# Optimization experiments

Hardware: AMD Instinct MI355X
Metric: run time of the kernel (lower is better)

## Reference

```python
import jax, jax.numpy as jnp
import numpy as np

B, S, HID = 1, 2048, 4096
H, KH, D = 32, 8, 128          # query heads, kv heads, head_dim
ROT = 64                       # rotary_dim = head_dim * partial_rotary_factor (0.5)
THETA = 10000.0
EPS = 1e-5
SCALE = D ** -0.5
NEG = -1e30


def setup_inputs() -> dict:
    key = jax.random.key(0)
    ks = jax.random.split(key, 7)
    return {
        "hidden_states": jax.random.normal(ks[0], (B, S, HID), jnp.float32),
        "Wq": jax.random.normal(ks[1], (H * D, HID), jnp.float32) * 0.02,
        "Wk": jax.random.normal(ks[2], (KH * D, HID), jnp.float32) * 0.02,
        "Wv": jax.random.normal(ks[3], (KH * D, HID), jnp.float32) * 0.02,
        "Wo": jax.random.normal(ks[4], (H * D, HID), jnp.float32).T.reshape(HID, H * D) * 0.02,
        "q_norm_w": jax.random.uniform(ks[5], (D,), jnp.float32),
        "k_norm_w": jax.random.uniform(ks[6], (D,), jnp.float32),
        "position_ids": jnp.arange(S, dtype=jnp.int32)[None, :],
    }


def rms_norm(x, w):
    # per-head RMSNorm in fp32, scale by (weight + 1)
    xf = x.astype(jnp.float32)
    var = jnp.mean(xf * xf, axis=-1, keepdims=True)
    return (xf * jax.lax.rsqrt(var + EPS) * (w.astype(jnp.float32) + 1.0)).astype(x.dtype)


def rope_cos_sin(position_ids):
    inv_freq = 1.0 / (THETA ** (jnp.arange(0, ROT, 2, dtype=jnp.float32) / ROT))
    freqs = position_ids.astype(jnp.float32)[..., None] * inv_freq  # [B,S,ROT/2]
    emb = jnp.concatenate([freqs, freqs], axis=-1)                  # [B,S,ROT]
    return jnp.cos(emb)[:, None], jnp.sin(emb)[:, None]             # [B,1,S,ROT]


def rotate_half(x):
    x1, x2 = jnp.split(x, 2, axis=-1)
    return jnp.concatenate([-x2, x1], axis=-1)


def apply_partial_rope(x, cos, sin):
    x_rot, x_pass = x[..., :ROT], x[..., ROT:]
    x_rot = x_rot * cos + rotate_half(x_rot) * sin
    return jnp.concatenate([x_rot, x_pass], axis=-1)


def reference(hidden_states, Wq, Wk, Wv, Wo, q_norm_w, k_norm_w, position_ids):
    # projections -> [B, heads, S, D]
    q = (hidden_states @ Wq.T).reshape(B, S, H, D).transpose(0, 2, 1, 3)
    k = (hidden_states @ Wk.T).reshape(B, S, KH, D).transpose(0, 2, 1, 3)
    v = (hidden_states @ Wv.T).reshape(B, S, KH, D).transpose(0, 2, 1, 3)

    q = rms_norm(q, q_norm_w)
    k = rms_norm(k, k_norm_w)

    cos, sin = rope_cos_sin(position_ids)
    q = apply_partial_rope(q, cos, sin)
    k = apply_partial_rope(k, cos, sin)

    # repeat kv heads (GQA) -> [B, H, S, D]
    rep = H // KH
    k = jnp.broadcast_to(k[:, :, None], (B, KH, rep, S, D)).reshape(B, H, S, D)
    v = jnp.broadcast_to(v[:, :, None], (B, KH, rep, S, D)).reshape(B, H, S, D)

    scores = jnp.einsum("bhqd,bhkd->bhqk", q, k) * SCALE
    causal = jnp.tril(jnp.ones((S, S), bool))
    scores = jnp.where(causal, scores, NEG)
    attn = jax.nn.softmax(scores, axis=-1)
    out = jnp.einsum("bhqk,bhkd->bhqd", attn, v)        # [B,H,S,D]
    out = out.transpose(0, 2, 1, 3).reshape(B, S, H * D)
    return out @ Wo.T                                    # [B,S,HID]
```

## Files before the change

### kernel.cpp

```cpp
#include <hip/hip_runtime.h>
#include <hip/hip_bf16.h>

#define AS1 __attribute__((address_space(1)))
#define AS3 __attribute__((address_space(3)))

typedef __attribute__((ext_vector_type(8))) short short8;
typedef __attribute__((ext_vector_type(4))) short short4v;
typedef __attribute__((ext_vector_type(4))) float f32x4;

constexpr int S_ = 2048;
constexpr int HID_ = 4096;
constexpr int NH = 32;
constexpr int NKH = 8;
constexpr float EPS_ = 1e-5f;
constexpr float SCALE_ = 0.08838834764831845f;

__device__ __forceinline__ short f2bf(float f) {
  __hip_bfloat16 h = __float2bfloat16(f);
  return *reinterpret_cast<short*>(&h);
}

__global__ __launch_bounds__(256) void cast_bf16_kernel(const float4* __restrict__ src,
                                                        short4v* __restrict__ dst, int n4) {
  int i = blockIdx.x * 256 + threadIdx.x;
  if (i >= n4) return;
  float4 v = src[i];
  short4v o;
  o[0] = f2bf(v.x); o[1] = f2bf(v.y); o[2] = f2bf(v.z); o[3] = f2bf(v.w);
  dst[i] = o;
}

__global__ __launch_bounds__(512, 2) void gemm8_bt(const short* __restrict__ A,
                                                   const short* __restrict__ B,
                                                   float* __restrict__ C,
                                                   int M, int N, int K) {
  extern __shared__ __align__(16) char smem[];
  const int t = threadIdx.x, w = t >> 6, lane = t & 63;
  const int nbx = N >> 8;
  int wg = blockIdx.x;
  const int cpx = gridDim.x >> 3;
  wg = (wg & 7) * cpx + (wg >> 3);
  const int by = wg / nbx, bx = wg % nbx;
  const long m0 = (long)by << 8, n0 = (long)bx << 8;
  const int wr = w >> 2, wc = w & 3;
  const int l15 = lane & 15, l4 = lane >> 4;
  const int NT = K >> 6;

  f32x4 acc[8][4];
#pragma unroll
  for (int f = 0; f < 8; ++f)
#pragma unroll
    for (int g = 0; g < 4; ++g) acc[f][g] = (f32x4){0.f, 0.f, 0.f, 0.f};

  auto STAGE = [&](int h) {
    int hm = h & (4 * NT - 1);
    int tt = hm >> 2, half = hm & 3;
    int buf = tt & 1;
    long k0 = (long)tt << 6;
    const short* src = (half < 2) ? A : B;
    long r0 = (half < 2) ? m0 : n0;
    char* lbase = smem + buf * 65536 + ((half >> 1) << 15) + ((half & 1) << 14);
#pragma unroll
    for (int j = 0; j < 2; ++j) {
      int row = ((half & 1) << 7) + j * 64 + w * 8 + (lane >> 3);
      int cs = (lane & 7) ^ (((row >> 2) & 1) << 1);
      __builtin_amdgcn_global_load_lds(
          (const AS1 void*)(src + (r0 + row) * K + k0 + cs * 8),
          (AS3 void*)(lbase + j * 8192 + w * 1024 + lane * 16), 16, 0, 0);
    }
  };
  auto LDA = [&](int buf, int f, int s) -> short8 {
    int ra = wr * 128 + f * 16 + l15;
    int byte = (ra * 128 + s * 64 + l4 * 16) ^ (((ra >> 2) & 1) << 5);
    return *(const short8*)(smem + buf * 65536 + byte);
  };
  auto LDB = [&](int buf, int g, int s) -> short8 {
    int rb = wc * 64 + g * 16 + l15;
    int byte = (rb * 128 + s * 64 + l4 * 16) ^ (((rb >> 2) & 1) << 5);
    return *(const short8*)(smem + buf * 65536 + 32768 + byte);
  };

#pragma unroll
  for (int h = 0; h < 8; ++h) STAGE(h);
  asm volatile("s_waitcnt vmcnt(8)" ::: "memory");
  asm volatile("s_barrier" ::: "memory");

  short8 af[4][2], bf2[4][2];
  for (int tt = 0; tt < NT; ++tt) {
    const int buf = tt & 1;
    const int p = tt * 4;
#pragma unroll
    for (int f = 0; f < 4; ++f) { af[f][0] = LDA(buf, f, 0); af[f][1] = LDA(buf, f, 1); }
#pragma unroll
    for (int g = 0; g < 2; ++g) { bf2[g][0] = LDB(buf, g, 0); bf2[g][1] = LDB(buf, g, 1); }
    if (tt) STAGE(p + 5);
    asm volatile("s_barrier" ::: "memory");
    __builtin_amdgcn_s_setprio(1);
#pragma unroll
    for (int f = 0; f < 4; ++f)
#pragma unroll
      for (int g = 0; g < 2; ++g) {
        acc[f][g] = __builtin_amdgcn_mfma_f32_16x16x32_bf16(af[f][0], bf2[g][0], acc[f][g], 0, 0, 0);
        acc[f][g] = __builtin_amdgcn_mfma_f32_16x16x32_bf16(af[f][1], bf2[g][1], acc[f][g], 0, 0, 0);
      }
    __builtin_amdgcn_s_setprio(0);
    asm volatile("s_barrier" ::: "memory");
#pragma unroll
    for (int g = 0; g < 2; ++g) { bf2[2 + g][0] = LDB(buf, 2 + g, 0); bf2[2 + g][1] = LDB(buf, 2 + g, 1); }
    if (tt) STAGE(p + 6);
    asm volatile("s_barrier" ::: "memory");
    __builtin_amdgcn_s_setprio(1);
#pragma unroll
    for (int f = 0; f < 4; ++f)
#pragma unroll
      for (int g = 0; g < 2; ++g) {
        acc[f][2 + g] = __builtin_amdgcn_mfma_f32_16x16x32_bf16(af[f][0], bf2[2 + g][0], acc[f][2 + g], 0, 0, 0);
        acc[f][2 + g] = __builtin_amdgcn_mfma_f32_16x16x32_bf16(af[f][1], bf2[2 + g][1], acc[f][2 + g], 0, 0, 0);
      }
    __builtin_amdgcn_s_setprio(0);
    asm volatile("s_barrier" ::: "memory");
#pragma unroll
    for (int f = 0; f < 4; ++f) { af[f][0] = LDA(buf, 4 + f, 0); af[f][1] = LDA(buf, 4 + f, 1); }
    if (tt) STAGE(p + 7);
    asm volatile("s_barrier" ::: "memory");
    __builtin_amdgcn_s_setprio(1);
#pragma unroll
    for (int f = 0; f < 4; ++f)
#pragma unroll
      for (int g = 0; g < 2; ++g) {
        acc[4 + f][g] = __builtin_amdgcn_mfma_f32_16x16x32_bf16(af[f][0], bf2[g][0], acc[4 + f][g], 0, 0, 0);
        acc[4 + f][g] = __builtin_amdgcn_mfma_f32_16x16x32_bf16(af[f][1], bf2[g][1], acc[4 + f][g], 0, 0, 0);
      }
    __builtin_amdgcn_s_setprio(0);
    asm volatile("s_barrier" ::: "memory");
    STAGE(p + 8);
    asm volatile("s_barrier" ::: "memory");
    __builtin_amdgcn_s_setprio(1);
#pragma unroll
    for (int f = 0; f < 4; ++f)
#pragma unroll
      for (int g = 0; g < 2; ++g) {
        acc[4 + f][2 + g] = __builtin_amdgcn_mfma_f32_16x16x32_bf16(af[f][0], bf2[2 + g][0], acc[4 + f][2 + g], 0, 0, 0);
        acc[4 + f][2 + g] = __builtin_amdgcn_mfma_f32_16x16x32_bf16(af[f][1], bf2[2 + g][1], acc[4 + f][2 + g], 0, 0, 0);
      }
    __builtin_amdgcn_s_setprio(0);
    asm volatile("s_waitcnt vmcnt(2)" ::: "memory");
    asm volatile("s_barrier" ::: "memory");
  }
#pragma unroll
  for (int f = 0; f < 8; ++f)
#pragma unroll
    for (int g = 0; g < 4; ++g)
#pragma unroll
      for (int r = 0; r < 4; ++r) {
        long m = m0 + wr * 128 + f * 16 + l4 * 4 + r;
        long n = n0 + wc * 64 + g * 16 + l15;
        C[m * N + n] = acc[f][g][r];
      }
}

__global__ __launch_bounds__(256) void normrope_kernel(const float* __restrict__ QKV,
    const int* __restrict__ pos_ids, const float* __restrict__ qw,
    const float* __restrict__ kw,
    short* __restrict__ Qn, short* __restrict__ Kn) {
  const int lane = threadIdx.x & 63;
  const long row = (long)blockIdx.x * 4 + (threadIdx.x >> 6);
  const long NQ = (long)S_ * NH;
  const float* src;
  short* dst;
  const float* wv;
  int s;
  float scl = 1.f;
  if (row < NQ) {
    s = (int)(row >> 5); int h = (int)(row & 31);
    src = QKV + (long)s * 6144 + h * 128;
    dst = Qn + ((long)h * S_ + s) * 128;
    wv = qw; scl = SCALE_;
  } else {
    long r2 = row - NQ; s = (int)(r2 >> 3); int kh = (int)(r2 & 7);
    src = QKV + (long)s * 6144 + 4096 + kh * 128;
    dst = Kn + ((long)kh * S_ + s) * 128;
    wv = kw;
  }
  float x0 = src[lane], x1 = src[lane + 64];
  float ss = x0 * x0 + x1 * x1;
#pragma unroll
  for (int m = 1; m < 64; m <<= 1) ss += __shfl_xor(ss, m);
  float inv = rsqrtf(ss * (1.f / 128.f) + EPS_);
  x0 = x0 * inv * (wv[lane] + 1.f);
  x1 = x1 * inv * (wv[lane + 64] + 1.f);
  int pos = pos_ids[s];
  int i = lane & 31;
  float invf = expf(-logf(10000.f) * ((float)(2 * i) / 64.f));
  float f = (float)pos * invf;
  float c = cosf(f), sn = sinf(f);
  float p = __shfl_xor(x0, 32);
  x0 = (lane < 32) ? (x0 * c - p * sn) : (x0 * c + p * sn);
  dst[lane] = f2bf(x0 * scl);
  dst[lane + 64] = f2bf(x1 * scl);
}

__global__ __launch_bounds__(256) void vtrans_kernel(const float* __restrict__ QKV,
                                                     short* __restrict__ Vt) {
  __shared__ __align__(16) float lt[64][68];
  const int t = threadIdx.x;
  const int s0 = blockIdx.x * 64, d0 = blockIdx.y * 64, kh = blockIdx.z;
  const float* src = QKV + (long)s0 * 6144 + 5120 + kh * 128 + d0;
#pragma unroll
  for (int i = 0; i < 4; ++i) {
    int idx = t + i * 256;
    int r = idx >> 4, c4 = (idx & 15) * 4;
    float4 v = *(const float4*)(src + (long)r * 6144 + c4);
    *(float4*)&lt[r][c4] = v;
  }
  __syncthreads();
  int d = t >> 2, seg = (t & 3) * 16;
  short* dst = Vt + ((long)kh * 128 + d0 + d) * S_ + s0 + seg;
  short8 a, b2;
#pragma unroll
  for (int j = 0; j < 8; ++j) a[j] = f2bf(lt[seg + j][d]);
#pragma unroll
  for (int j = 0; j < 8; ++j) b2[j] = f2bf(lt[seg + 8 + j][d]);
  *(short8*)dst = a;
  *(short8*)(dst + 8) = b2;
}

__global__ __launch_bounds__(512, 2) void attn_kernel(const short* __restrict__ Qn,
    const short* __restrict__ Kn, const short* __restrict__ Vt,
    short* __restrict__ O) {
  __shared__ __align__(16) short Ks[64 * 128];
  __shared__ __align__(16) short Vs[128 * 64];
  __shared__ __align__(16) short Ps[8][16 * 64];
  const int t = threadIdx.x, w = t >> 6, lane = t & 63;
  const int b = blockIdx.x;
  const int h = b & 31, qt = 15 - (b >> 5);
  const int kh = h >> 2;
  const int q0 = qt * 128;
  const int l15 = lane & 15, lk = (lane >> 4) * 8;

  short8 qf[4];
  {
    const short* Qh = Qn + ((long)h * S_ + q0 + w * 16) * 128;
#pragma unroll
    for (int ks = 0; ks < 4; ++ks)
      qf[ks] = *(const short8*)(Qh + l15 * 128 + ks * 32 + lk);
  }
  f32x4 o[8];
#pragma unroll
  for (int nf = 0; nf < 8; ++nf) o[nf] = (f32x4){0.f, 0.f, 0.f, 0.f};
  float mrun[4], lrun[4];
#pragma unroll
  for (int r = 0; r < 4; ++r) { mrun[r] = -1e30f; lrun[r] = 0.f; }

  const short* Khp = Kn + (long)kh * S_ * 128;
  const short* Vtp = Vt + (long)kh * 128 * S_;

  const int krr = w * 8 + (lane >> 4);
  const int kc = lane & 15;
  const int vdd = w * 16 + (lane >> 3);
  const int vc = lane & 7;
  char* pw = (char*)Ps[w];
  const int mrow = (lane >> 4) * 4;

  for (int kv0 = 0; kv0 < q0 + 128; kv0 += 64) {
#pragma unroll
    for (int j = 0; j < 2; ++j) {
      int rr = krr + j * 4;
      __builtin_amdgcn_global_load_lds(
          (const AS1 void*)(Khp + (long)(kv0 + rr) * 128 + ((kc ^ (rr & 7)) * 8)),
          (AS3 void*)(Ks + (w * 8 + j * 4) * 128 + lane * 8), 16, 0, 0);
    }
#pragma unroll
    for (int j = 0; j < 2; ++j) {
      int d = vdd + j * 8;
      __builtin_amdgcn_global_load_lds(
          (const AS1 void*)(Vtp + (long)d * S_ + kv0 + ((vc ^ (d & 7)) * 8)),
          (AS3 void*)(Vs + (w * 16 + j * 8) * 64 + lane * 8), 16, 0, 0);
    }
    __syncthreads();

    const bool active = (kv0 <= q0 + w * 16 + 15);
    if (active) {
      f32x4 sc[4];
#pragma unroll
      for (int ni = 0; ni < 4; ++ni) sc[ni] = (f32x4){0.f, 0.f, 0.f, 0.f};
#pragma unroll
      for (int ks = 0; ks < 4; ++ks)
#pragma unroll
        for (int ni = 0; ni < 4; ++ni) {
          int row = ni * 16 + l15;
          int bb = row * 256 + (ks * 32 + lk) * 2; bb ^= (row & 7) << 4;
          short8 kf = *(const short8*)((const char*)Ks + bb);
          sc[ni] = __builtin_amdgcn_mfma_f32_16x16x32_bf16(qf[ks], kf, sc[ni], 0, 0, 0);
        }
      if (kv0 + 64 > q0 + w * 16) {
#pragma unroll
        for (int ni = 0; ni < 4; ++ni)
#pragma unroll
          for (int r = 0; r < 4; ++r) {
            int qm = q0 + w * 16 + mrow + r;
            int kcol = kv0 + ni * 16 + l15;
            if (kcol > qm) sc[ni][r] = -1e30f;
          }
      }
      short pb[4][4];
#pragma unroll
      for (int r = 0; r < 4; ++r) {
        float mx = fmaxf(fmaxf(sc[0][r], sc[1][r]), fmaxf(sc[2][r], sc[3][r]));
        mx = fmaxf(mx, __shfl_xor(mx, 1));
        mx = fmaxf(mx, __shfl_xor(mx, 2));
        mx = fmaxf(mx, __shfl_xor(mx, 4));
        mx = fmaxf(mx, __shfl_xor(mx, 8));
        float mnew = fmaxf(mrun[r], mx);
        float scale = expf(mrun[r] - mnew);
        mrun[r] = mnew;
        float ssum = 0.f;
#pragma unroll
        for (int ni = 0; ni < 4; ++ni) {
          float p = expf(sc[ni][r] - mnew);
          ssum += p;
          pb[ni][r] = f2bf(p);
        }
        ssum += __shfl_xor(ssum, 1);
        ssum += __shfl_xor(ssum, 2);
        ssum += __shfl_xor(ssum, 4);
        ssum += __shfl_xor(ssum, 8);
        lrun[r] = lrun[r] * scale + ssum;
#pragma unroll
        for (int nf = 0; nf < 8; ++nf) o[nf][r] *= scale;
      }
#pragma unroll
      for (int ni = 0; ni < 4; ++ni)
#pragma unroll
        for (int r = 0; r < 4; ++r) {
          int m = mrow + r;
          int bb = m * 128 + (ni * 16 + l15) * 2; bb ^= (m & 7) << 4;
          *(short*)(pw + bb) = pb[ni][r];
        }
#pragma unroll
      for (int ks2 = 0; ks2 < 2; ++ks2) {
        int bp = l15 * 128 + (ks2 * 32 + lk) * 2; bp ^= (l15 & 7) << 4;
        short8 pf = *(const short8*)(pw + bp);
#pragma unroll
        for (int nf = 0; nf < 8; ++nf) {
          int bv = (nf * 16 + l15) * 128 + (ks2 * 32 + lk) * 2; bv ^= (l15 & 7) << 4;
          short8 vf = *(const short8*)((const char*)Vs + bv);
          o[nf] = __builtin_amdgcn_mfma_f32_16x16x32_bf16(pf, vf, o[nf], 0, 0, 0);
        }
      }
    }
    __syncthreads();
  }
#pragma unroll
  for (int r = 0; r < 4; ++r) {
    float invl = 1.f / lrun[r];
    int m = q0 + w * 16 + mrow + r;
#pragma unroll
    for (int nf = 0; nf < 8; ++nf)
      O[(long)m * 4096 + h * 128 + nf * 16 + l15] = f2bf(o[nf][r] * invl);
  }
}

extern "C" void kernel_launch(void* const* d_in, const int* in_sizes, int n_in,
                              void* d_out, int out_size, void* d_ws, size_t ws_size,
                              hipStream_t stream) {
  const float* hidden = (const float*)d_in[0];
  const float* Wq = (const float*)d_in[1];
  const float* Wk = (const float*)d_in[2];
  const float* Wv = (const float*)d_in[3];
  const float* Wo = (const float*)d_in[4];
  const float* qw = (const float*)d_in[5];
  const float* kw = (const float*)d_in[6];
  const int* pos = (const int*)d_in[7];
  float* out = (float*)d_out;

  char* ws = (char*)d_ws;
  short* hid_bf  = (short*)(ws + 0);
  short* Wqkv_bf = (short*)(ws + 16777216L);
  short* Wo_bf   = (short*)(ws + 67108864L);
  float* QKVf    = (float*)(ws + 100663296L);
  short* Qn      = (short*)(ws + 150994944L);
  short* Kn      = (short*)(ws + 167772160L);
  short* Vt      = (short*)(ws + 171966464L);
  short* AO      = hid_bf;

  (void)hipFuncSetAttribute((const void*)gemm8_bt,
                            hipFuncAttributeMaxDynamicSharedMemorySize, 131072);

  auto cast = [&](const float* s_, short* d_, long n) {
    int n4 = (int)(n / 4);
    cast_bf16_kernel<<<(n4 + 255) / 256, 256, 0, stream>>>((const float4*)s_, (short4v*)d_, n4);
  };
  cast(hidden, hid_bf, (long)S_ * HID_);
  cast(Wq, Wqkv_bf, (long)4096 * 4096);
  cast(Wk, Wqkv_bf + (long)4096 * 4096, (long)1024 * 4096);
  cast(Wv, Wqkv_bf + (long)5120 * 4096, (long)1024 * 4096);
  cast(Wo, Wo_bf, (long)4096 * 4096);

  gemm8_bt<<<dim3(192), 512, 131072, stream>>>(hid_bf, Wqkv_bf, QKVf, S_, 6144, HID_);

  normrope_kernel<<<(S_ * (NH + NKH)) / 4, 256, 0, stream>>>(QKVf, pos, qw, kw, Qn, Kn);
  vtrans_kernel<<<dim3(S_ / 64, 2, NKH), 256, 0, stream>>>(QKVf, Vt);
  attn_kernel<<<dim3(512), 512, 0, stream>>>(Qn, Kn, Vt, AO);

  gemm8_bt<<<dim3(128), 512, 131072, stream>>>(AO, Wo_bf, out, S_, HID_, HID_);
}
```

Measured before the change: 602.8 us.

## Template GEMM on N-tile width to fill all CUs with 256 workgroups

The bf16 GEMM is templated on the N tile width (G*64 columns). The QKV projection now uses 256x192 tiles and the output projection 256x128 tiles, so both launch 256 workgroups instead of 192 and 128, aiming to keep all compute units busy. The LDS swizzle moves to a full 8-way XOR on row&7, and the staging schedule is rewritten around per-tile units. Smaller tiles lower per-block arithmetic intensity and add global traffic.

```diff
diff --git a/kernel.cpp b/kernel.cpp
--- a/kernel.cpp
+++ b/kernel.cpp
@@ -30,118 +30,131 @@
   dst[i] = o;
 }
 
+template <int G>
 __global__ __launch_bounds__(512, 2) void gemm8_bt(const short* __restrict__ A,
                                                    const short* __restrict__ B,
                                                    float* __restrict__ C,
                                                    int M, int N, int K) {
+  constexpr int BN = G * 64;
+  constexpr int BUFSZ = 32768 + G * 8192;
+  constexpr int GH = (G + 1) / 2;
   extern __shared__ __align__(16) char smem[];
   const int t = threadIdx.x, w = t >> 6, lane = t & 63;
-  const int nbx = N >> 8;
+  const int nbx = N / BN;
   int wg = blockIdx.x;
   const int cpx = gridDim.x >> 3;
   wg = (wg & 7) * cpx + (wg >> 3);
   const int by = wg / nbx, bx = wg % nbx;
-  const long m0 = (long)by << 8, n0 = (long)bx << 8;
+  const long m0 = (long)by * 256, n0 = (long)bx * BN;
   const int wr = w >> 2, wc = w & 3;
   const int l15 = lane & 15, l4 = lane >> 4;
   const int NT = K >> 6;
 
-  f32x4 acc[8][4];
+  f32x4 acc[8][G];
 #pragma unroll
   for (int f = 0; f < 8; ++f)
 #pragma unroll
-    for (int g = 0; g < 4; ++g) acc[f][g] = (f32x4){0.f, 0.f, 0.f, 0.f};
-
-  auto STAGE = [&](int h) {
-    int hm = h & (4 * NT - 1);
-    int tt = hm >> 2, half = hm & 3;
-    int buf = tt & 1;
-    long k0 = (long)tt << 6;
-    const short* src = (half < 2) ? A : B;
-    long r0 = (half < 2) ? m0 : n0;
-    char* lbase = smem + buf * 65536 + ((half >> 1) << 15) + ((half & 1) << 14);
-#pragma unroll
-    for (int j = 0; j < 2; ++j) {
-      int row = ((half & 1) << 7) + j * 64 + w * 8 + (lane >> 3);
-      int cs = (lane & 7) ^ (((row >> 2) & 1) << 1);
+    for (int g = 0; g < G; ++g) acc[f][g] = (f32x4){0.f, 0.f, 0.f, 0.f};
+
+  const int srow = w * 8 + (lane >> 3);
+  const int schunk = lane & 7;
+
+  auto STAGE = [&](int tile, int unit) {
+    int tb = tile & (NT - 1);
+    long k0 = (long)tb << 6;
+    char* base = smem + (tb & 1) * BUFSZ;
+    if (unit < 2) {
+#pragma unroll
+      for (int j = 0; j < 2; ++j) {
+        int row = unit * 128 + j * 64 + srow;
+        int ch = schunk ^ (row & 7);
+        __builtin_amdgcn_global_load_lds(
+            (const AS1 void*)(A + (m0 + row) * K + k0 + ch * 8),
+            (AS3 void*)(base + unit * 16384 + j * 8192 + w * 1024 + lane * 16), 16, 0, 0);
+      }
+    } else {
+      int bj = unit - 2;
+      int row = bj * 64 + srow;
+      int ch = schunk ^ (row & 7);
       __builtin_amdgcn_global_load_lds(
-          (const AS1 void*)(src + (r0 + row) * K + k0 + cs * 8),
-          (AS3 void*)(lbase + j * 8192 + w * 1024 + lane * 16), 16, 0, 0);
+          (const AS1 void*)(B + (n0 + row) * K + k0 + ch * 8),
+          (AS3 void*)(base + 32768 + bj * 8192 + w * 1024 + lane * 16), 16, 0, 0);
     }
   };
   auto LDA = [&](int buf, int f, int s) -> short8 {
     int ra = wr * 128 + f * 16 + l15;
-    int byte = (ra * 128 + s * 64 + l4 * 16) ^ (((ra >> 2) & 1) << 5);
-    return *(const short8*)(smem + buf * 65536 + byte);
+    int byte = ra * 128 + (((s << 2) + l4) ^ (ra & 7)) * 16;
+    return *(const short8*)(smem + buf * BUFSZ + byte);
   };
   auto LDB = [&](int buf, int g, int s) -> short8 {
-    int rb = wc * 64 + g * 16 + l15;
-    int byte = (rb * 128 + s * 64 + l4 * 16) ^ (((rb >> 2) & 1) << 5);
-    return *(const short8*)(smem + buf * 65536 + 32768 + byte);
+    int rb = wc * (G * 16) + g * 16 + l15;
+    int byte = 32768 + rb * 128 + (((s << 2) + l4) ^ (rb & 7)) * 16;
+    return *(const short8*)(smem + buf * BUFSZ + byte);
   };
 
 #pragma unroll
-  for (int h = 0; h < 8; ++h) STAGE(h);
-  asm volatile("s_waitcnt vmcnt(8)" ::: "memory");
+  for (int u = 0; u < 2 + G; ++u) STAGE(0, u);
+  STAGE(1, 0);
+  asm volatile("s_waitcnt vmcnt(2)" ::: "memory");
   asm volatile("s_barrier" ::: "memory");
 
-  short8 af[4][2], bf2[4][2];
+  short8 af[4][2], bf2[G][2];
   for (int tt = 0; tt < NT; ++tt) {
     const int buf = tt & 1;
-    const int p = tt * 4;
 #pragma unroll
     for (int f = 0; f < 4; ++f) { af[f][0] = LDA(buf, f, 0); af[f][1] = LDA(buf, f, 1); }
 #pragma unroll
-    for (int g = 0; g < 2; ++g) { bf2[g][0] = LDB(buf, g, 0); bf2[g][1] = LDB(buf, g, 1); }
-    if (tt) STAGE(p + 5);
+    for (int g = 0; g < GH; ++g) { bf2[g][0] = LDB(buf, g, 0); bf2[g][1] = LDB(buf, g, 1); }
+    STAGE(tt + 1, 1);
     asm volatile("s_barrier" ::: "memory");
     __builtin_amdgcn_s_setprio(1);
 #pragma unroll
     for (int f = 0; f < 4; ++f)
 #pragma unroll
-      for (int g = 0; g < 2; ++g) {
+      for (int g = 0; g < GH; ++g) {
         acc[f][g] = __builtin_amdgcn_mfma_f32_16x16x32_bf16(af[f][0], bf2[g][0], acc[f][g], 0, 0, 0);
         acc[f][g] = __builtin_amdgcn_mfma_f32_16x16x32_bf16(af[f][1], bf2[g][1], acc[f][g], 0, 0, 0);
       }
     __builtin_amdgcn_s_setprio(0);
     asm volatile("s_barrier" ::: "memory");
 #pragma unroll
-    for (int g = 0; g < 2; ++g) { bf2[2 + g][0] = LDB(buf, 2 + g, 0); bf2[2 + g][1] = LDB(buf, 2 + g, 1); }
-    if (tt) STAGE(p + 6);
+    for (int g = GH; g < G; ++g) { bf2[g][0] = LDB(buf, g, 0); bf2[g][1] = LDB(buf, g, 1); }
+#pragma unroll
+    for (int u = 2; u < G + 1; ++u) STAGE(tt + 1, u);
     asm volatile("s_barrier" ::: "memory");
     __builtin_amdgcn_s_setprio(1);
 #pragma unroll
     for (int f = 0; f < 4; ++f)
 #pragma unroll
-      for (int g = 0; g < 2; ++g) {
-        acc[f][2 + g] = __builtin_amdgcn_mfma_f32_16x16x32_bf16(af[f][0], bf2[2 + g][0], acc[f][2 + g], 0, 0, 0);
-        acc[f][2 + g] = __builtin_amdgcn_mfma_f32_16x16x32_bf16(af[f][1], bf2[2 + g][1], acc[f][2 + g], 0, 0, 0);
+      for (int g = GH; g < G; ++g) {
+        acc[f][g] = __builtin_amdgcn_mfma_f32_16x16x32_bf16(af[f][0], bf2[g][0], acc[f][g], 0, 0, 0);
+        acc[f][g] = __builtin_amdgcn_mfma_f32_16x16x32_bf16(af[f][1], bf2[g][1], acc[f][g], 0, 0, 0);
       }
     __builtin_amdgcn_s_setprio(0);
     asm volatile("s_barrier" ::: "memory");
 #pragma unroll
     for (int f = 0; f < 4; ++f) { af[f][0] = LDA(buf, 4 + f, 0); af[f][1] = LDA(buf, 4 + f, 1); }
-    if (tt) STAGE(p + 7);
+    STAGE(tt + 1, G + 1);
     asm volatile("s_barrier" ::: "memory");
     __builtin_amdgcn_s_setprio(1);
 #pragma unroll
     for (int f = 0; f < 4; ++f)
 #pragma unroll
-      for (int g = 0; g < 2; ++g) {
+      for (int g = 0; g < GH; ++g) {
         acc[4 + f][g] = __builtin_amdgcn_mfma_f32_16x16x32_bf16(af[f][0], bf2[g][0], acc[4 + f][g], 0, 0, 0);
         acc[4 + f][g] = __builtin_amdgcn_mfma_f32_16x16x32_bf16(af[f][1], bf2[g][1], acc[4 + f][g], 0, 0, 0);
       }
     __builtin_amdgcn_s_setprio(0);
     asm volatile("s_barrier" ::: "memory");
-    STAGE(p + 8);
+    STAGE(tt + 2, 0);
     asm volatile("s_barrier" ::: "memory");
     __builtin_amdgcn_s_setprio(1);
 #pragma unroll
     for (int f = 0; f < 4; ++f)
 #pragma unroll
-      for (int g = 0; g < 2; ++g) {
-        acc[4 + f][2 + g] = __builtin_amdgcn_mfma_f32_16x16x32_bf16(af[f][0], bf2[2 + g][0], acc[4 + f][2 + g], 0, 0, 0);
-        acc[4 + f][2 + g] = __builtin_amdgcn_mfma_f32_16x16x32_bf16(af[f][1], bf2[2 + g][1], acc[4 + f][2 + g], 0, 0, 0);
+      for (int g = GH; g < G; ++g) {
+        acc[4 + f][g] = __builtin_amdgcn_mfma_f32_16x16x32_bf16(af[f][0], bf2[g][0], acc[4 + f][g], 0, 0, 0);
+        acc[4 + f][g] = __builtin_amdgcn_mfma_f32_16x16x32_bf16(af[f][1], bf2[g][1], acc[4 + f][g], 0, 0, 0);
       }
     __builtin_amdgcn_s_setprio(0);
     asm volatile("s_waitcnt vmcnt(2)" ::: "memory");
@@ -150,11 +163,11 @@
 #pragma unroll
   for (int f = 0; f < 8; ++f)
 #pragma unroll
-    for (int g = 0; g < 4; ++g)
+    for (int g = 0; g < G; ++g)
 #pragma unroll
       for (int r = 0; r < 4; ++r) {
         long m = m0 + wr * 128 + f * 16 + l4 * 4 + r;
-        long n = n0 + wc * 64 + g * 16 + l15;
+        long n = n0 + wc * (G * 16) + g * 16 + l15;
         C[m * N + n] = acc[f][g][r];
       }
 }
@@ -384,8 +397,10 @@
   short* Vt      = (short*)(ws + 171966464L);
   short* AO      = hid_bf;
 
-  (void)hipFuncSetAttribute((const void*)gemm8_bt,
-                            hipFuncAttributeMaxDynamicSharedMemorySize, 131072);
+  (void)hipFuncSetAttribute((const void*)gemm8_bt<3>,
+                            hipFuncAttributeMaxDynamicSharedMemorySize, 114688);
+  (void)hipFuncSetAttribute((const void*)gemm8_bt<2>,
+                            hipFuncAttributeMaxDynamicSharedMemorySize, 98304);
 
   auto cast = [&](const float* s_, short* d_, long n) {
     int n4 = (int)(n / 4);
@@ -397,11 +412,11 @@
   cast(Wv, Wqkv_bf + (long)5120 * 4096, (long)1024 * 4096);
   cast(Wo, Wo_bf, (long)4096 * 4096);
 
-  gemm8_bt<<<dim3(192), 512, 131072, stream>>>(hid_bf, Wqkv_bf, QKVf, S_, 6144, HID_);
+  gemm8_bt<3><<<dim3(256), 512, 114688, stream>>>(hid_bf, Wqkv_bf, QKVf, S_, 6144, HID_);
 
   normrope_kernel<<<(S_ * (NH + NKH)) / 4, 256, 0, stream>>>(QKVf, pos, qw, kw, Qn, Kn);
   vtrans_kernel<<<dim3(S_ / 64, 2, NKH), 256, 0, stream>>>(QKVf, Vt);
   attn_kernel<<<dim3(512), 512, 0, stream>>>(Qn, Kn, Vt, AO);
 
-  gemm8_bt<<<dim3(128), 512, 131072, stream>>>(AO, Wo_bf, out, S_, HID_, HID_);
-}
+  gemm8_bt<2><<<dim3(256), 512, 98304, stream>>>(AO, Wo_bf, out, S_, HID_, HID_);
+}
```

New measurement: 524.4 us. 1.15x faster.
